# Kernel tuning notes

Hardware: AMD Instinct MI355X
Metric: run time of the kernel (lower is better)

## Reference

```python
import jax, jax.numpy as jnp
import numpy as np

EPS = 1e-8

def setup_inputs() -> dict:
    key = jax.random.key(0)
    ks = jax.random.split(key, 5)
    N, Cin, Cout, K, H, W = 16, 512, 512, 3, 64, 64
    return {
        "x": jax.random.normal(ks[0], (N, Cin, H, W), dtype=jnp.float32),
        "s": jax.random.normal(ks[1], (N, Cin), dtype=jnp.float32),
        "noise": jax.random.normal(ks[2], (N, Cout, H, W), dtype=jnp.float32),
        "w": jax.random.normal(ks[3], (Cout, Cin, K, K), dtype=jnp.float32),
        "b": jax.random.normal(ks[4], (Cout,), dtype=jnp.float32),
    }

def reference(x, s, noise, w, b):
    # Demodulation coefficient: d[n,o] = rsqrt(sum_{c,kh,kw} (w[o,c]*s[n,c])^2 + eps)
    # einsum: (s^2)[n,c] . (w^2 summed over kh,kw)[o,c] -> [n,o]
    w2 = jnp.sum(w * w, axis=(2, 3))                      # [Cout, Cin]
    d = jax.lax.rsqrt(jnp.einsum('nc,oc->no', s * s, w2) + EPS)  # [N, Cout]
    # Fold per-sample modulation into the input, demodulation into the output
    # (mathematically identical to grouped conv with per-sample modulated weights).
    x_mod = x * s[:, :, None, None]                       # [N, Cin, H, W]
    y = jax.lax.conv_general_dilated(
        x_mod, w,
        window_strides=(1, 1),
        padding='SAME',
        dimension_numbers=('NCHW', 'OIHW', 'NCHW'),
    )                                                     # [N, Cout, H, W]
    y = y * d[:, :, None, None] + b[None, :, None, None] + noise
    return jnp.where(y >= 0, y, 0.2 * y)  # LeakyReLU(0.2)
```

## Files before the change

### kernel.cpp

```cpp
#include <hip/hip_runtime.h>
#include <cstdint>
#include <cstddef>

typedef __attribute__((ext_vector_type(8))) short bf16x8;
typedef __attribute__((ext_vector_type(4))) float floatx4;

#define NBATCH 16
#define CIN    512
#define COUT   512
#define HH     64
#define WW     64
#define HP     66
#define XSLOT  72
#define XSZ    (4 * 66 * XSLOT)
#define ASZ    (128 * XSLOT)

static __device__ __forceinline__ unsigned short f2bf(float f) {
  union { float f; unsigned u; } cv; cv.f = f;
  unsigned u = cv.u;
  return (unsigned short)((u + 0x7FFFu + ((u >> 16) & 1u)) >> 16);
}

__global__ void k_wprep(const float* __restrict__ w, unsigned short* __restrict__ wr,
                        float* __restrict__ w2t) {
  int o = blockIdx.x;
  int c = blockIdx.y * 256 + threadIdx.x;
  const float* wp = w + ((size_t)o * CIN + c) * 9;
  float v[9]; float sum = 0.f;
#pragma unroll
  for (int r = 0; r < 9; ++r) { v[r] = wp[r]; sum += v[r] * v[r]; }
  w2t[(size_t)c * COUT + o] = sum;
#pragma unroll
  for (int r = 0; r < 9; ++r)
    wr[((size_t)r * COUT + o) * CIN + c] = f2bf(v[r]);
}

__global__ void k_dcoef(const float* __restrict__ s, const float* __restrict__ w2t,
                        float* __restrict__ d) {
  __shared__ float s2[CIN];
  int n = blockIdx.y;
  int o = blockIdx.x * 256 + threadIdx.x;
  for (int c = threadIdx.x; c < CIN; c += 256) {
    float sv = s[n * CIN + c]; s2[c] = sv * sv;
  }
  __syncthreads();
  float sum = 0.f;
  for (int c = 0; c < CIN; ++c) sum += s2[c] * w2t[(size_t)c * COUT + o];
  d[n * COUT + o] = rsqrtf(sum + 1e-8f);
}

__global__ void k_xmod(const float* __restrict__ x, const float* __restrict__ s,
                       unsigned short* __restrict__ xmp) {
  __shared__ __align__(16) unsigned short tile[WW * 520];
  int tid  = threadIdx.x;
  int n    = blockIdx.x >> 6;
  int h    = blockIdx.x & 63;
  int wcol = tid & 63;
  int grp  = tid >> 6;
#pragma unroll
  for (int i = 0; i < 16; ++i) {
    int c0 = (i * 4 + grp) * 8;
    bf16x8 pk;
#pragma unroll
    for (int j = 0; j < 8; ++j) {
      int c = c0 + j;
      float v = x[(((size_t)n * CIN + c) * HH + h) * WW + wcol] * s[n * CIN + c];
      pk[j] = (short)f2bf(v);
    }
    *(bf16x8*)(tile + wcol * 520 + c0) = pk;
  }
  __syncthreads();
#pragma unroll
  for (int i = 0; i < 16; ++i) {
    int wv = i * 4 + grp;
    bf16x8 v = *(const bf16x8*)(tile + wv * 520 + wcol * 8);
    *(bf16x8*)(xmp + (((size_t)n * HP + (h + 1)) * HP + (wv + 1)) * CIN + wcol * 8) = v;
  }
}

__global__ __launch_bounds__(256, 2)
void k_conv(const unsigned short* __restrict__ xmp, const unsigned short* __restrict__ wr,
            const float* __restrict__ d, const float* __restrict__ bias,
            const float* __restrict__ noise, float* __restrict__ out) {
  __shared__ __align__(16) unsigned short smem[XSZ + ASZ];
  unsigned short* Xs = smem;
  unsigned short* As = smem + XSZ;

  int tid  = threadIdx.x;
  int lane = tid & 63;
  int l15  = lane & 15;
  int quad = lane >> 4;
  int wv   = tid >> 6;
  int wrow = wv & 1;
  int woc  = wv >> 1;

  int bx  = blockIdx.x;
  int n   = bx >> 5;
  int h0  = (bx & 31) * 2;
  int ocb = blockIdx.y * 128;

  floatx4 acc[4][4];
#pragma unroll
  for (int a = 0; a < 4; ++a)
#pragma unroll
    for (int b = 0; b < 4; ++b)
#pragma unroll
      for (int q = 0; q < 4; ++q) acc[a][b][q] = 0.f;

  for (int cb = 0; cb < 8; ++cb) {
    int c0 = cb * 64;
    {
      bf16x8 xv[8];
#pragma unroll
      for (int i = 0; i < 8; ++i) {
        int idx = i * 256 + tid;
        int row = idx / 528;
        int rem = idx - row * 528;
        int col = rem >> 3, ch = rem & 7;
        xv[i] = *(const bf16x8*)(xmp + (((size_t)n * HP + (h0 + row)) * HP + col) * CIN + c0 + ch * 8);
      }
#pragma unroll
      for (int i = 0; i < 8; ++i) {
        int idx = i * 256 + tid;
        int row = idx / 528;
        int rem = idx - row * 528;
        int col = rem >> 3, ch = rem & 7;
        *(bf16x8*)(Xs + (row * 66 + col) * XSLOT + ch * 8) = xv[i];
      }
      if (tid < 64) {
        int rem = 464 + tid;
        int col = rem >> 3, ch = rem & 7;
        bf16x8 v = *(const bf16x8*)(xmp + (((size_t)n * HP + (h0 + 3)) * HP + col) * CIN + c0 + ch * 8);
        *(bf16x8*)(Xs + (3 * 66 + col) * XSLOT + ch * 8) = v;
      }
    }
#pragma unroll
    for (int i = 0; i < 4; ++i) {
      int idx = i * 256 + tid;
      int ol = idx >> 3, ch = idx & 7;
      bf16x8 v = *(const bf16x8*)(wr + ((size_t)(ocb + ol)) * CIN + c0 + ch * 8);
      *(bf16x8*)(As + ol * XSLOT + ch * 8) = v;
    }
    __syncthreads();

    for (int r = 0; r < 9; ++r) {
      bf16x8 wpre[4];
      if (r < 8) {
#pragma unroll
        for (int i = 0; i < 4; ++i) {
          int idx = i * 256 + tid;
          int ol = idx >> 3, ch = idx & 7;
          wpre[i] = *(const bf16x8*)(wr + ((size_t)((r + 1) * COUT) + ocb + ol) * CIN + c0 + ch * 8);
        }
      }
      int kh = r / 3;
      int kw = r - kh * 3;
      int xrow = wrow + kh;
#pragma unroll
      for (int ks = 0; ks < 2; ++ks) {
        bf16x8 af[4], bfv[4];
#pragma unroll
        for (int mf = 0; mf < 4; ++mf)
          af[mf] = *(const bf16x8*)(As + (woc * 64 + mf * 16 + l15) * XSLOT + ks * 32 + quad * 8);
#pragma unroll
        for (int nf = 0; nf < 4; ++nf)
          bfv[nf] = *(const bf16x8*)(Xs + (xrow * 66 + (nf * 16 + l15 + kw)) * XSLOT + ks * 32 + quad * 8);
#pragma unroll
        for (int mf = 0; mf < 4; ++mf)
#pragma unroll
          for (int nf = 0; nf < 4; ++nf)
            acc[mf][nf] = __builtin_amdgcn_mfma_f32_16x16x32_bf16(af[mf], bfv[nf], acc[mf][nf], 0, 0, 0);
      }
      __syncthreads();
      if (r < 8) {
#pragma unroll
        for (int i = 0; i < 4; ++i) {
          int idx = i * 256 + tid;
          int ol = idx >> 3, ch = idx & 7;
          *(bf16x8*)(As + ol * XSLOT + ch * 8) = wpre[i];
        }
        __syncthreads();
      }
    }
  }

  int h = h0 + wrow;
#pragma unroll
  for (int mf = 0; mf < 4; ++mf) {
#pragma unroll
    for (int i = 0; i < 4; ++i) {
      int o = ocb + woc * 64 + mf * 16 + quad * 4 + i;
      float dd = d[n * COUT + o];
      float bb = bias[o];
      size_t base = (((size_t)n * COUT + o) * HH + h) * WW;
#pragma unroll
      for (int nf = 0; nf < 4; ++nf) {
        int wc = nf * 16 + l15;
        float v = acc[mf][nf][i] * dd + bb + noise[base + wc];
        out[base + wc] = (v >= 0.f) ? v : 0.2f * v;
      }
    }
  }
}

extern "C" void kernel_launch(void* const* d_in, const int* in_sizes, int n_in,
                              void* d_out, int out_size, void* d_ws, size_t ws_size,
                              hipStream_t stream) {
  (void)in_sizes; (void)n_in; (void)out_size; (void)ws_size;
  const float* x     = (const float*)d_in[0];
  const float* s     = (const float*)d_in[1];
  const float* noise = (const float*)d_in[2];
  const float* w     = (const float*)d_in[3];
  const float* bias  = (const float*)d_in[4];
  float* out = (float*)d_out;

  char* ws = (char*)d_ws;
  const size_t XMP_BYTES = (size_t)NBATCH * HP * HP * CIN * 2;
  const size_t WR_BYTES  = (size_t)9 * COUT * CIN * 2;
  const size_t W2_BYTES  = (size_t)CIN * COUT * 4;
  unsigned short* xmp = (unsigned short*)ws;
  unsigned short* wrr = (unsigned short*)(ws + XMP_BYTES);
  float* w2t          = (float*)(ws + XMP_BYTES + WR_BYTES);
  float* dcoef        = (float*)(ws + XMP_BYTES + WR_BYTES + W2_BYTES);

  hipMemsetAsync(xmp, 0, XMP_BYTES, stream);
  k_wprep<<<dim3(COUT, 2),  256, 0, stream>>>(w, wrr, w2t);
  k_dcoef<<<dim3(2, NBATCH), 256, 0, stream>>>(s, w2t, dcoef);
  k_xmod <<<dim3(NBATCH * HH), 256, 0, stream>>>(x, s, xmp);
  k_conv <<<dim3(NBATCH * HH / 2, COUT / 128), 256, 0, stream>>>(xmp, wrr, dcoef, bias, noise, out);
}
```

Baseline: 686.1 us.

## Load conv weight fragments directly from global and drop LDS weight staging

The conv kernel no longer stages weight tiles in LDS. Each wave now reads its MFMA A-fragments straight from global memory, which removes the per-tap LDS store and the two barriers around it, and the smaller LDS footprint lets the occupancy target rise from 2 to 3 blocks. The full memset of the padded input is replaced by a kernel that zeroes only the halo cells, and the demodulation coefficient kernel splits the channel reduction across more threads and blocks. The risk is that the direct global weight loads, which go through cache, add latency and traffic in the inner MFMA loop.

```diff
diff --git a/kernel.cpp b/kernel.cpp
--- a/kernel.cpp
+++ b/kernel.cpp
@@ -13,12 +13,26 @@
 #define HP     66
 #define XSLOT  72
 #define XSZ    (4 * 66 * XSLOT)
-#define ASZ    (128 * XSLOT)
 
 static __device__ __forceinline__ unsigned short f2bf(float f) {
   union { float f; unsigned u; } cv; cv.f = f;
   unsigned u = cv.u;
   return (unsigned short)((u + 0x7FFFu + ((u >> 16) & 1u)) >> 16);
+}
+
+__global__ void k_halo(unsigned short* __restrict__ xmp) {
+  int idx = blockIdx.x * 256 + threadIdx.x;
+  if (idx >= NBATCH * 260 * 64) return;
+  int ch   = idx & 63;
+  int cell = (idx >> 6) % 260;
+  int n    = (idx >> 6) / 260;
+  int h, w;
+  if      (cell < 66)  { h = 0;              w = cell;       }
+  else if (cell < 132) { h = 65;             w = cell - 66;  }
+  else if (cell < 196) { h = cell - 132 + 1; w = 0;          }
+  else                 { h = cell - 196 + 1; w = 65;         }
+  uint4 z = {0u, 0u, 0u, 0u};
+  *(uint4*)(xmp + (((size_t)n * HP + h) * HP + w) * CIN + ch * 8) = z;
 }
 
 __global__ void k_wprep(const float* __restrict__ w, unsigned short* __restrict__ wr,
@@ -38,15 +52,27 @@
 __global__ void k_dcoef(const float* __restrict__ s, const float* __restrict__ w2t,
                         float* __restrict__ d) {
   __shared__ float s2[CIN];
-  int n = blockIdx.y;
-  int o = blockIdx.x * 256 + threadIdx.x;
+  __shared__ float partial[4][64];
+  int n  = blockIdx.y;
+  int ol = threadIdx.x & 63;
+  int cg = threadIdx.x >> 6;
+  int o  = blockIdx.x * 64 + ol;
   for (int c = threadIdx.x; c < CIN; c += 256) {
     float sv = s[n * CIN + c]; s2[c] = sv * sv;
   }
   __syncthreads();
   float sum = 0.f;
-  for (int c = 0; c < CIN; ++c) sum += s2[c] * w2t[(size_t)c * COUT + o];
-  d[n * COUT + o] = rsqrtf(sum + 1e-8f);
+#pragma unroll 8
+  for (int i = 0; i < 128; ++i) {
+    int c = cg * 128 + i;
+    sum += s2[c] * w2t[(size_t)c * COUT + o];
+  }
+  partial[cg][ol] = sum;
+  __syncthreads();
+  if (cg == 0) {
+    float t = partial[0][ol] + partial[1][ol] + partial[2][ol] + partial[3][ol];
+    d[n * COUT + o] = rsqrtf(t + 1e-8f);
+  }
 }
 
 __global__ void k_xmod(const float* __restrict__ x, const float* __restrict__ s,
@@ -78,13 +104,11 @@
   }
 }
 
-__global__ __launch_bounds__(256, 2)
+__global__ __launch_bounds__(256, 3)
 void k_conv(const unsigned short* __restrict__ xmp, const unsigned short* __restrict__ wr,
             const float* __restrict__ d, const float* __restrict__ bias,
             const float* __restrict__ noise, float* __restrict__ out) {
-  __shared__ __align__(16) unsigned short smem[XSZ + ASZ];
-  unsigned short* Xs = smem;
-  unsigned short* As = smem + XSZ;
+  __shared__ __align__(16) unsigned short Xs[XSZ];
 
   int tid  = threadIdx.x;
   int lane = tid & 63;
@@ -99,6 +123,8 @@
   int h0  = (bx & 31) * 2;
   int ocb = blockIdx.y * 128;
 
+  const unsigned short* wrl = wr + ((size_t)(ocb + woc * 64 + l15)) * CIN + quad * 8;
+
   floatx4 acc[4][4];
 #pragma unroll
   for (int a = 0; a < 4; ++a)
@@ -109,78 +135,59 @@
 
   for (int cb = 0; cb < 8; ++cb) {
     int c0 = cb * 64;
-    {
-      bf16x8 xv[8];
-#pragma unroll
-      for (int i = 0; i < 8; ++i) {
-        int idx = i * 256 + tid;
-        int row = idx / 528;
-        int rem = idx - row * 528;
-        int col = rem >> 3, ch = rem & 7;
-        xv[i] = *(const bf16x8*)(xmp + (((size_t)n * HP + (h0 + row)) * HP + col) * CIN + c0 + ch * 8);
-      }
-#pragma unroll
-      for (int i = 0; i < 8; ++i) {
-        int idx = i * 256 + tid;
-        int row = idx / 528;
-        int rem = idx - row * 528;
-        int col = rem >> 3, ch = rem & 7;
-        *(bf16x8*)(Xs + (row * 66 + col) * XSLOT + ch * 8) = xv[i];
-      }
-      if (tid < 64) {
-        int rem = 464 + tid;
-        int col = rem >> 3, ch = rem & 7;
-        bf16x8 v = *(const bf16x8*)(xmp + (((size_t)n * HP + (h0 + 3)) * HP + col) * CIN + c0 + ch * 8);
-        *(bf16x8*)(Xs + (3 * 66 + col) * XSLOT + ch * 8) = v;
-      }
-    }
-#pragma unroll
-    for (int i = 0; i < 4; ++i) {
+    bf16x8 xv[8], xt;
+#pragma unroll
+    for (int i = 0; i < 8; ++i) {
       int idx = i * 256 + tid;
-      int ol = idx >> 3, ch = idx & 7;
-      bf16x8 v = *(const bf16x8*)(wr + ((size_t)(ocb + ol)) * CIN + c0 + ch * 8);
-      *(bf16x8*)(As + ol * XSLOT + ch * 8) = v;
+      int row = idx / 528;
+      int rem = idx - row * 528;
+      int col = rem >> 3, ch = rem & 7;
+      xv[i] = *(const bf16x8*)(xmp + (((size_t)n * HP + (h0 + row)) * HP + col) * CIN + c0 + ch * 8);
+    }
+    if (tid < 64) {
+      int rem = 464 + tid;
+      int col = rem >> 3, ch = rem & 7;
+      xt = *(const bf16x8*)(xmp + (((size_t)n * HP + (h0 + 3)) * HP + col) * CIN + c0 + ch * 8);
     }
     __syncthreads();
-
+#pragma unroll
+    for (int i = 0; i < 8; ++i) {
+      int idx = i * 256 + tid;
+      int row = idx / 528;
+      int rem = idx - row * 528;
+      int col = rem >> 3, ch = rem & 7;
+      *(bf16x8*)(Xs + (row * 66 + col) * XSLOT + ch * 8) = xv[i];
+    }
+    if (tid < 64) {
+      int rem = 464 + tid;
+      int col = rem >> 3, ch = rem & 7;
+      *(bf16x8*)(Xs + (3 * 66 + col) * XSLOT + ch * 8) = xt;
+    }
+    __syncthreads();
+
+#pragma unroll
     for (int r = 0; r < 9; ++r) {
-      bf16x8 wpre[4];
-      if (r < 8) {
-#pragma unroll
-        for (int i = 0; i < 4; ++i) {
-          int idx = i * 256 + tid;
-          int ol = idx >> 3, ch = idx & 7;
-          wpre[i] = *(const bf16x8*)(wr + ((size_t)((r + 1) * COUT) + ocb + ol) * CIN + c0 + ch * 8);
-        }
-      }
       int kh = r / 3;
       int kw = r - kh * 3;
       int xrow = wrow + kh;
-#pragma unroll
-      for (int ks = 0; ks < 2; ++ks) {
-        bf16x8 af[4], bfv[4];
+      bf16x8 af[2][4], bfv[2][4];
+#pragma unroll
+      for (int ks = 0; ks < 2; ++ks)
 #pragma unroll
         for (int mf = 0; mf < 4; ++mf)
-          af[mf] = *(const bf16x8*)(As + (woc * 64 + mf * 16 + l15) * XSLOT + ks * 32 + quad * 8);
+          af[ks][mf] = *(const bf16x8*)(wrl + ((size_t)r * COUT + mf * 16) * CIN + c0 + ks * 32);
+#pragma unroll
+      for (int ks = 0; ks < 2; ++ks)
 #pragma unroll
         for (int nf = 0; nf < 4; ++nf)
-          bfv[nf] = *(const bf16x8*)(Xs + (xrow * 66 + (nf * 16 + l15 + kw)) * XSLOT + ks * 32 + quad * 8);
+          bfv[ks][nf] = *(const bf16x8*)(Xs + (xrow * 66 + (nf * 16 + l15 + kw)) * XSLOT + ks * 32 + quad * 8);
+#pragma unroll
+      for (int ks = 0; ks < 2; ++ks)
 #pragma unroll
         for (int mf = 0; mf < 4; ++mf)
 #pragma unroll
           for (int nf = 0; nf < 4; ++nf)
-            acc[mf][nf] = __builtin_amdgcn_mfma_f32_16x16x32_bf16(af[mf], bfv[nf], acc[mf][nf], 0, 0, 0);
-      }
-      __syncthreads();
-      if (r < 8) {
-#pragma unroll
-        for (int i = 0; i < 4; ++i) {
-          int idx = i * 256 + tid;
-          int ol = idx >> 3, ch = idx & 7;
-          *(bf16x8*)(As + ol * XSLOT + ch * 8) = wpre[i];
-        }
-        __syncthreads();
-      }
+            acc[mf][nf] = __builtin_amdgcn_mfma_f32_16x16x32_bf16(af[ks][mf], bfv[ks][nf], acc[mf][nf], 0, 0, 0);
     }
   }
 
@@ -223,9 +230,9 @@
   float* w2t          = (float*)(ws + XMP_BYTES + WR_BYTES);
   float* dcoef        = (float*)(ws + XMP_BYTES + WR_BYTES + W2_BYTES);
 
-  hipMemsetAsync(xmp, 0, XMP_BYTES, stream);
+  k_halo <<<dim3((NBATCH * 260 * 64 + 255) / 256), 256, 0, stream>>>(xmp);
   k_wprep<<<dim3(COUT, 2),  256, 0, stream>>>(w, wrr, w2t);
-  k_dcoef<<<dim3(2, NBATCH), 256, 0, stream>>>(s, w2t, dcoef);
+  k_dcoef<<<dim3(COUT / 64, NBATCH), 256, 0, stream>>>(s, w2t, dcoef);
   k_xmod <<<dim3(NBATCH * HH), 256, 0, stream>>>(x, s, xmp);
   k_conv <<<dim3(NBATCH * HH / 2, COUT / 128), 256, 0, stream>>>(xmp, wrr, dcoef, bias, noise, out);
 }
```

Result: slower. 980.5 us (+42.9%).
